# Kernel tuning notes

Hardware: AMD Instinct MI355X
Metric: run time of the kernel (lower is better)

## Reference

```python
import jax, jax.numpy as jnp
import numpy as np

B, T, D = 2, 2048, 2048
H, K, Hd = 16, 8, 128
EPS = 1e-6
THETA = 1e6


def _rms_norm(x, w):
    # x: [..., Hd]
    return x * jax.lax.rsqrt(jnp.mean(x * x, axis=-1, keepdims=True) + EPS) * w


def _rope(x, sin, cos):
    # x: [B, T, Hh, Hd]; sin/cos: [T, Hd//2]
    s = sin[None, :, None, :]
    c = cos[None, :, None, :]
    x1 = x[..., 0::2]
    x2 = x[..., 1::2]
    # NOTE: source concatenates halves (non-interleaved output), replicate exactly
    return jnp.concatenate([x1 * c - x2 * s, x1 * s + x2 * c], axis=-1)


def setup_inputs() -> dict:
    key = jax.random.key(0)
    ks = jax.random.split(key, 5)
    scale = 0.02
    x = jax.random.normal(ks[0], (B, T, D), dtype=jnp.float32)
    Wq = jax.random.normal(ks[1], (D, H * Hd), dtype=jnp.float32) * scale
    Wk = jax.random.normal(ks[2], (D, K * Hd), dtype=jnp.float32) * scale
    Wv = jax.random.normal(ks[3], (D, K * Hd), dtype=jnp.float32) * scale
    Wo = jax.random.normal(ks[4], (H * Hd, D), dtype=jnp.float32) * scale
    qn_w = jnp.ones((Hd,), dtype=jnp.float32)
    kn_w = jnp.ones((Hd,), dtype=jnp.float32)
    # RotaryEmbedding: inv_freq = theta**(-arange(0,Hd,2)/Hd); freqs = outer(t, inv_freq)
    inv_freq = 1.0 / (THETA ** (jnp.arange(0, Hd, 2, dtype=jnp.float32) / Hd))
    freqs = jnp.arange(T, dtype=jnp.float32)[:, None] * inv_freq[None, :]
    return {"x": x, "Wq": Wq, "Wk": Wk, "Wv": Wv, "Wo": Wo,
            "qn_w": qn_w, "kn_w": kn_w,
            "sin": jnp.sin(freqs), "cos": jnp.cos(freqs)}


def reference(x, Wq, Wk, Wv, Wo, qn_w, kn_w, sin, cos):
    Bx, Tx, _ = x.shape
    q = (x @ Wq).reshape(Bx, Tx, H, Hd)
    k = (x @ Wk).reshape(Bx, Tx, K, Hd)
    v = (x @ Wv).reshape(Bx, Tx, K, Hd)
    q = _rope(_rms_norm(q, qn_w), sin, cos)
    k = _rope(_rms_norm(k, kn_w), sin, cos)
    q = q.transpose(0, 2, 1, 3)  # [B,H,T,Hd]
    k = k.transpose(0, 2, 1, 3)  # [B,K,T,Hd]
    v = v.transpose(0, 2, 1, 3)
    if K != 1 and K != H:
        rep = H // K
        k = jnp.repeat(k, rep, axis=1)  # repeat_interleave on head dim
        v = jnp.repeat(v, rep, axis=1)
    att = jnp.einsum('bhqd,bhkd->bhqk', q.astype(jnp.float32),
                     k.astype(jnp.float32)) / np.sqrt(Hd).astype(np.float32)
    causal = jnp.tril(jnp.ones((Tx, Tx), dtype=bool))
    att = jnp.where(causal[None, None], att, -jnp.inf)
    att = jax.nn.softmax(att, axis=-1)
    out = jnp.einsum('bhqk,bhkd->bhqd', att, v.astype(jnp.float32))
    out = out.astype(q.dtype).transpose(0, 2, 1, 3).reshape(Bx, Tx, H * Hd)
    return out @ Wo
```

## Files before the change

kernel.cpp:

```cpp
#include <hip/hip_runtime.h>
#include <stdint.h>


#define B_ 2
#define T_ 2048
#define D_ 2048
#define H_ 16
#define KH_ 8
#define HD_ 128
#define M_ (B_*T_)
#define NQKV_ 4096
#define QK_SCALE_LOG2E 0.1275174337f

typedef unsigned short u16;
typedef unsigned int   u32;
typedef __attribute__((ext_vector_type(8)))  __bf16 bf16x8_t;
typedef __attribute__((ext_vector_type(4)))  float  f32x4_t;
typedef __attribute__((ext_vector_type(16))) float  f32x16_t;
typedef __attribute__((ext_vector_type(4)))  u32    u32x4_t;

__device__ __forceinline__ u16 f2bf(float f) {
    u32 x = __float_as_uint(f);
    return (u16)((x + 0x7fffu + ((x >> 16) & 1u)) >> 16);
}
__device__ __forceinline__ u32 pack2(u16 a, u16 b) { return (u32)a | ((u32)b << 16); }

__device__ __forceinline__ void gload16(const void* g, void* l) {
    __builtin_amdgcn_global_load_lds(
        (__attribute__((address_space(1))) const void*)(unsigned long long)g,
        (__attribute__((address_space(3))) void*)(u32)(unsigned long long)l,
        16, 0, 0);
}

__global__ void cast_x_kernel(const float* __restrict__ in, u16* __restrict__ out) {
    int i = (blockIdx.x * 256 + threadIdx.x) * 4;
    float4 v = *(const float4*)(in + i);
    u32 lo = pack2(f2bf(v.x), f2bf(v.y));
    u32 hi = pack2(f2bf(v.z), f2bf(v.w));
    *(uint2*)(out + i) = make_uint2(lo, hi);
}

__global__ void tcast_kernel(const float* __restrict__ in, u16* __restrict__ out,
                             int ncols) {
    __shared__ u16 tile[64][65];
    int k0 = blockIdx.x * 64;
    int n0 = blockIdx.y * 64;
    int tid = threadIdx.x;
#pragma unroll
    for (int i = 0; i < 8; ++i) {
        int idx = tid + i * 256;
        int r = idx >> 5, c2 = idx & 31;
        float2 v = *(const float2*)(in + (size_t)(k0 + r) * ncols + n0 + 2 * c2);
        tile[r][2 * c2]     = f2bf(v.x);
        tile[r][2 * c2 + 1] = f2bf(v.y);
    }
    __syncthreads();
#pragma unroll
    for (int i = 0; i < 8; ++i) {
        int idx = tid + i * 256;
        int rn = idx >> 5, c2 = idx & 31;
        *(u32*)(out + (size_t)(n0 + rn) * 2048 + k0 + 2 * c2) =
            pack2(tile[2 * c2][rn], tile[2 * c2 + 1][rn]);
    }
}

__global__ void __launch_bounds__(256)
gemm_kernel(const u16* __restrict__ A, const u16* __restrict__ Bt,
            float* __restrict__ C, int N) {
    __shared__ u16 As[128 * 32];
    __shared__ u16 Bs[128 * 32];
    const int tid  = threadIdx.x;
    const int lane = tid & 63;
    const int wid  = tid >> 6;
    const int m0 = blockIdx.x * 128;
    const int n0 = blockIdx.y * 128;

    const int c0 = wid * 2, c1 = wid * 2 + 1;
    const int r0 = c0 * 16 + (lane >> 2);
    const int r1 = c1 * 16 + (lane >> 2);
    const int cl = lane & 3;
    const int g0 = cl ^ ((r0 >> 1) & 3);
    const int g1 = cl ^ ((r1 >> 1) & 3);
    const u16* gA0 = A  + (size_t)(m0 + r0) * 2048 + g0 * 8;
    const u16* gA1 = A  + (size_t)(m0 + r1) * 2048 + g1 * 8;
    const u16* gB0 = Bt + (size_t)(n0 + r0) * 2048 + g0 * 8;
    const u16* gB1 = Bt + (size_t)(n0 + r1) * 2048 + g1 * 8;
    u16* lA0 = As + c0 * 512;
    u16* lA1 = As + c1 * 512;
    u16* lB0 = Bs + c0 * 512;
    u16* lB1 = Bs + c1 * 512;

    const int wm = (wid >> 1) * 64, wn = (wid & 1) * 64;
    const int fr  = lane & 15;
    const int kg  = lane >> 4;

    f32x4_t acc[4][4];
#pragma unroll
    for (int m = 0; m < 4; ++m)
#pragma unroll
        for (int n = 0; n < 4; ++n)
#pragma unroll
            for (int j = 0; j < 4; ++j) acc[m][n][j] = 0.0f;

    for (int ks = 0; ks < 64; ++ks) {
        gload16(gA0, lA0); gload16(gA1, lA1);
        gload16(gB0, lB0); gload16(gB1, lB1);
        gA0 += 32; gA1 += 32; gB0 += 32; gB1 += 32;
        __syncthreads();
        bf16x8_t af[4], bfv[4];
#pragma unroll
        for (int m = 0; m < 4; ++m) {
            int row = wm + m * 16 + fr;
            int phys = kg ^ ((row >> 1) & 3);
            af[m] = *(const bf16x8_t*)(As + row * 32 + phys * 8);
        }
#pragma unroll
        for (int n = 0; n < 4; ++n) {
            int row = wn + n * 16 + fr;
            int phys = kg ^ ((row >> 1) & 3);
            bfv[n] = *(const bf16x8_t*)(Bs + row * 32 + phys * 8);
        }
#pragma unroll
        for (int m = 0; m < 4; ++m)
#pragma unroll
            for (int n = 0; n < 4; ++n)
                acc[m][n] = __builtin_amdgcn_mfma_f32_16x16x32_bf16(
                    af[m], bfv[n], acc[m][n], 0, 0, 0);
        __syncthreads();
    }

#pragma unroll
    for (int m = 0; m < 4; ++m)
#pragma unroll
        for (int n = 0; n < 4; ++n) {
            int col   = n0 + wn + n * 16 + fr;
            int rbase = m0 + wm + m * 16 + kg * 4;
#pragma unroll
            for (int j = 0; j < 4; ++j)
                C[(size_t)(rbase + j) * N + col] = acc[m][n][j];
        }
}

__global__ void __launch_bounds__(256)
normrope_kernel(const float* __restrict__ Cqkv,
                const float* __restrict__ qw, const float* __restrict__ kw,
                const float* __restrict__ sinT, const float* __restrict__ cosT,
                u16* __restrict__ qbf, u16* __restrict__ kbf, u16* __restrict__ vbf) {
    int lane = threadIdx.x & 63;
    int w    = threadIdx.x >> 6;
    int rid  = blockIdx.x * 4 + w;
    int m   = rid >> 5;
    int sub = rid & 31;
    int b = m >> 11, t = m & (T_ - 1);

    if (sub >= 24) {
        int kh = sub - 24;
        float2 x = *(const float2*)(Cqkv + (size_t)m * NQKV_ + 3072 + kh * HD_ + 2 * lane);
        *(u32*)(vbf + ((size_t)(b * KH_ + kh) * T_ + t) * HD_ + 2 * lane) =
            pack2(f2bf(x.x), f2bf(x.y));
        return;
    }
    bool isq = sub < 16;
    int  hh  = isq ? sub : sub - 16;
    int  colbase = isq ? hh * HD_ : 2048 + hh * HD_;
    float2 x = *(const float2*)(Cqkv + (size_t)m * NQKV_ + colbase + 2 * lane);
    float ss = x.x * x.x + x.y * x.y;
#pragma unroll
    for (int sh = 1; sh < 64; sh <<= 1) ss += __shfl_xor(ss, sh, 64);
    float scale = rsqrtf(ss * (1.0f / 128.0f) + 1e-6f);
    const float* wp = isq ? qw : kw;
    float2 wv = *(const float2*)(wp + 2 * lane);
    float y1 = x.x * scale * wv.x;
    float y2 = x.y * scale * wv.y;
    float c = cosT[t * 64 + lane], s = sinT[t * 64 + lane];
    float oa = y1 * c - y2 * s;
    float ob = y1 * s + y2 * c;
    if (isq) { oa *= QK_SCALE_LOG2E; ob *= QK_SCALE_LOG2E; }
    u16* outp = isq ? (qbf + ((size_t)(b * H_  + hh) * T_ + t) * HD_)
                    : (kbf + ((size_t)(b * KH_ + hh) * T_ + t) * HD_);
    outp[lane]      = f2bf(oa);
    outp[64 + lane] = f2bf(ob);
}

__global__ void vtrans_kernel(const u16* __restrict__ in, u16* __restrict__ out) {
    __shared__ u16 tile[64][65];
    int t0 = blockIdx.x * 64;
    int d0 = blockIdx.y * 64;
    size_t bi = (size_t)blockIdx.z * T_ * HD_;
    size_t bo = (size_t)blockIdx.z * HD_ * T_;
    int tid = threadIdx.x;
#pragma unroll
    for (int i = 0; i < 8; ++i) {
        int idx = tid + i * 256;
        int r = idx >> 5, c2 = idx & 31;
        u32 v = *(const u32*)(in + bi + (size_t)(t0 + r) * HD_ + d0 + 2 * c2);
        tile[r][2 * c2]     = (u16)(v & 0xffffu);
        tile[r][2 * c2 + 1] = (u16)(v >> 16);
    }
    __syncthreads();
#pragma unroll
    for (int i = 0; i < 8; ++i) {
        int idx = tid + i * 256;
        int rd = idx >> 5, c2 = idx & 31;
        *(u32*)(out + bo + (size_t)(d0 + rd) * T_ + t0 + 2 * c2) =
            pack2(tile[2 * c2][rd], tile[2 * c2 + 1][rd]);
    }
}

__global__ void __launch_bounds__(256, 2)
attn_kernel(const u16* __restrict__ qg, const u16* __restrict__ kgl,
            const u16* __restrict__ vtg, u16* __restrict__ attout) {
    __shared__ u16 Kt[2][64 * 128];
    __shared__ u16 Vt[2][128 * 64];

    const int tid = threadIdx.x, lane = tid & 63, w = tid >> 6;
    const int qb = (int)gridDim.x - 1 - (int)blockIdx.x;
    const int h = blockIdx.y, b = blockIdx.z;
    const int kh = h >> 1;
    const int q0 = qb * 128;
    const int col = lane & 31;
    const int hi  = lane >> 5;
    const int l7  = lane & 7;
    const int l15 = lane & 15;
    const int qw0 = q0 + w * 32;
    const int qlane = qw0 + col;

    const u16* qbase = qg  + ((size_t)(b * H_  + h ) * T_) * HD_;
    const u16* kbase = kgl + ((size_t)(b * KH_ + kh) * T_) * HD_;
    const u16* vbase = vtg + ((size_t)(b * KH_ + kh) * HD_) * T_;

    bf16x8_t qf[8];
#pragma unroll
    for (int s = 0; s < 8; ++s)
        qf[s] = *(const bf16x8_t*)(qbase + (size_t)qlane * HD_ + s * 16 + hi * 8);

    const int krl = lane >> 4, kcl = lane & 15;
    const int vrl = lane >> 3, vcl = lane & 7;

    f32x16_t o[4];
#pragma unroll
    for (int dt = 0; dt < 4; ++dt)
#pragma unroll
        for (int r = 0; r < 16; ++r) o[dt][r] = 0.0f;
    float mrow = -1e30f, lrow = 0.0f;

    const int nt = 2 * (qb + 1);

#define STAGE(buf, tt)                                                          \
    do {                                                                        \
        int kv0s = (tt) * 64;                                                   \
        _Pragma("unroll")                                                       \
        for (int cc = 0; cc < 4; ++cc) {                                        \
            int c = w * 4 + cc;                                                 \
            int r = c * 4 + krl;                                                \
            gload16(kbase + (size_t)(kv0s + r) * HD_ + (kcl ^ (r & 15)) * 8,    \
                    &Kt[buf][c * 512]);                                         \
            int rv = c * 8 + vrl;                                               \
            gload16(vbase + (size_t)rv * T_ + kv0s + (vcl ^ (rv & 7)) * 8,      \
                    &Vt[buf][c * 512]);                                         \
        }                                                                       \
    } while (0)

    STAGE(0, 0);
    __syncthreads();

    for (int t = 0; t < nt; ++t) {
        const int cur = t & 1;
        const int kv0 = t * 64;
        if (t + 1 < nt) STAGE(cur ^ 1, t + 1);

        if (kv0 <= qw0 + 31) {
            f32x16_t s0, s1;
#pragma unroll
            for (int r = 0; r < 16; ++r) { s0[r] = 0.0f; s1[r] = 0.0f; }
            __builtin_amdgcn_s_setprio(1);
#pragma unroll
            for (int ss = 0; ss < 8; ++ss) {
                bf16x8_t kf0 = *(const bf16x8_t*)
                    (&Kt[cur][col * 128 + (((2 * ss + hi) ^ l15) * 8)]);
                s0 = __builtin_amdgcn_mfma_f32_32x32x16_bf16(kf0, qf[ss], s0, 0, 0, 0);
                bf16x8_t kf1 = *(const bf16x8_t*)
                    (&Kt[cur][(32 + col) * 128 + (((2 * ss + hi) ^ l15) * 8)]);
                s1 = __builtin_amdgcn_mfma_f32_32x32x16_bf16(kf1, qf[ss], s1, 0, 0, 0);
            }
            __builtin_amdgcn_s_setprio(0);
            if (kv0 + 63 > qw0) {
#pragma unroll
                for (int r = 0; r < 16; ++r) {
                    int cr = (r & 3) + 8 * (r >> 2) + 4 * hi;
                    if (kv0 + cr      > qlane) s0[r] = -1e30f;
                    if (kv0 + 32 + cr > qlane) s1[r] = -1e30f;
                }
            }
            float tmax = s0[0];
#pragma unroll
            for (int r = 1; r < 16; ++r) tmax = fmaxf(tmax, s0[r]);
#pragma unroll
            for (int r = 0; r < 16; ++r) tmax = fmaxf(tmax, s1[r]);
            tmax = fmaxf(tmax, __shfl_xor(tmax, 32, 64));
            float mnew = fmaxf(mrow, tmax);
            float corr = exp2f(mrow - mnew);
            mrow = mnew;
            float ps = 0.0f;
#pragma unroll
            for (int r = 0; r < 16; ++r) {
                s0[r] = exp2f(s0[r] - mrow); ps += s0[r];
                s1[r] = exp2f(s1[r] - mrow); ps += s1[r];
            }
            lrow = lrow * corr + ps;
#pragma unroll
            for (int dt = 0; dt < 4; ++dt)
#pragma unroll
                for (int r = 0; r < 16; ++r) o[dt][r] *= corr;
            u32 pd0[8], pd1[8], po0[8], po1[8];
#pragma unroll
            for (int i = 0; i < 8; ++i) {
                pd0[i] = pack2(f2bf(s0[2 * i]), f2bf(s0[2 * i + 1]));
                pd1[i] = pack2(f2bf(s1[2 * i]), f2bf(s1[2 * i + 1]));
                po0[i] = __shfl_xor(pd0[i], 32, 64);
                po1[i] = __shfl_xor(pd1[i], 32, 64);
            }
            bf16x8_t pf[4];
#pragma unroll
            for (int ks = 0; ks < 4; ++ks) {
                const u32* pd = (ks < 2) ? pd0 : pd1;
                const u32* po = (ks < 2) ? po0 : po1;
                int base = (ks & 1) * 4;
                union { u32 u[4]; bf16x8_t v; } f;
                f.u[0] = hi ? po[base + 2] : pd[base + 0];
                f.u[1] = hi ? po[base + 3] : pd[base + 1];
                f.u[2] = hi ? pd[base + 2] : po[base + 0];
                f.u[3] = hi ? pd[base + 3] : po[base + 1];
                pf[ks] = f.v;
            }
            __builtin_amdgcn_s_setprio(1);
#pragma unroll
            for (int dt = 0; dt < 4; ++dt) {
                int dl = dt * 32 + col;
#pragma unroll
                for (int ks = 0; ks < 4; ++ks) {
                    bf16x8_t vf = *(const bf16x8_t*)
                        (&Vt[cur][dl * 64 + (((2 * ks + hi) ^ l7) * 8)]);
                    o[dt] = __builtin_amdgcn_mfma_f32_32x32x16_bf16(vf, pf[ks], o[dt], 0, 0, 0);
                }
            }
            __builtin_amdgcn_s_setprio(0);
        }
        __syncthreads();
    }
#undef STAGE

    float ltot = lrow + __shfl_xor(lrow, 32, 64);
    float inv  = 1.0f / ltot;
    u16* Tr = &Kt[0][0] + w * 4096;
#pragma unroll
    for (int dt = 0; dt < 4; ++dt)
#pragma unroll
        for (int g = 0; g < 4; ++g) {
            int slot = ((dt << 2) | g) ^ (col & 7);
            u32 lo  = pack2(f2bf(o[dt][4 * g + 0] * inv), f2bf(o[dt][4 * g + 1] * inv));
            u32 hi2 = pack2(f2bf(o[dt][4 * g + 2] * inv), f2bf(o[dt][4 * g + 3] * inv));
            *(uint2*)(Tr + col * 128 + slot * 8 + 4 * hi) = make_uint2(lo, hi2);
        }
    size_t rowbase = (size_t)(b * T_ + qw0);
#pragma unroll
    for (int p = 0; p < 8; ++p) {
        int ql   = p * 4 + (lane >> 4);
        int slot = lane & 15;
        int dl   = (slot ^ (ql & 7)) * 8;
        u32x4_t v = *(const u32x4_t*)(Tr + ql * 128 + slot * 8);
        *(u32x4_t*)(attout + (rowbase + ql) * 2048 + h * HD_ + dl) = v;
    }
}

extern "C" void kernel_launch(void* const* d_in, const int* in_sizes, int n_in,
                              void* d_out, int out_size, void* d_ws, size_t ws_size,
                              hipStream_t stream) {
    const float* x    = (const float*)d_in[0];
    const float* Wq   = (const float*)d_in[1];
    const float* Wk   = (const float*)d_in[2];
    const float* Wv   = (const float*)d_in[3];
    const float* Wo   = (const float*)d_in[4];
    const float* qw   = (const float*)d_in[5];
    const float* kw   = (const float*)d_in[6];
    const float* sinT = (const float*)d_in[7];
    const float* cosT = (const float*)d_in[8];
    float* out = (float*)d_out;

    u16*  x_bf   = (u16*)d_ws;
    u16*  wqkv_t = x_bf   + (size_t)M_ * D_;
    u16*  wo_t   = wqkv_t + (size_t)4096 * 2048;
    float* c_qkv = (float*)(wo_t + (size_t)2048 * 2048);
    u16*  q_bf   = (u16*)(c_qkv + (size_t)M_ * NQKV_);
    u16*  k_bf   = q_bf + (size_t)B_ * H_  * T_ * HD_;
    u16*  v_bf   = k_bf + (size_t)B_ * KH_ * T_ * HD_;
    u16*  v_t    = v_bf + (size_t)B_ * KH_ * T_ * HD_;
    u16*  att_bf = v_t  + (size_t)B_ * KH_ * T_ * HD_;

    cast_x_kernel<<<(M_ * D_) / 1024, 256, 0, stream>>>(x, x_bf);
    tcast_kernel<<<dim3(32, 32), 256, 0, stream>>>(Wq, wqkv_t, 2048);
    tcast_kernel<<<dim3(32, 16), 256, 0, stream>>>(Wk, wqkv_t + (size_t)2048 * 2048, 1024);
    tcast_kernel<<<dim3(32, 16), 256, 0, stream>>>(Wv, wqkv_t + (size_t)3072 * 2048, 1024);
    tcast_kernel<<<dim3(32, 32), 256, 0, stream>>>(Wo, wo_t, 2048);

    gemm_kernel<<<dim3(32, 32), 256, 0, stream>>>(x_bf, wqkv_t, c_qkv, 4096);
    normrope_kernel<<<(M_ * 32) / 4, 256, 0, stream>>>(c_qkv, qw, kw, sinT, cosT,
                                                       q_bf, k_bf, v_bf);
    vtrans_kernel<<<dim3(32, 2, 16), 256, 0, stream>>>(v_bf, v_t);
    attn_kernel<<<dim3(16, 16, 2), 256, 0, stream>>>(q_bf, k_bf, v_t, att_bf);
    gemm_kernel<<<dim3(32, 16), 256, 0, stream>>>(att_bf, wo_t, out, 2048);
}
```

Before: 415.0 us.

## Replace GEMM with 256x256-tile 8-wave double-buffered pipelined kernel

Replaces the 128x128, single-buffered GEMM with a 256x256-tile, 512-thread kernel. It double-buffers A and B in LDS and splits each K step into four phases, so global loads for later tiles overlap with MFMA work, using sched barriers, s_setprio and explicit vmcnt waits. The larger tile raises data reuse per loaded byte and the deeper pipeline hides memory latency. The cost is much more LDS (128KB per block) and registers, lower occupancy, and far fewer blocks (256 and 128), which may underfill the GPU's compute units.

```diff
diff --git a/kernel.cpp b/kernel.cpp
--- a/kernel.cpp
+++ b/kernel.cpp
@@ -64,80 +64,140 @@
     }
 }
 
-__global__ void __launch_bounds__(256)
-gemm_kernel(const u16* __restrict__ A, const u16* __restrict__ Bt,
-            float* __restrict__ C, int N) {
-    __shared__ u16 As[128 * 32];
-    __shared__ u16 Bs[128 * 32];
+#define NKT 32
+
+__global__ void __launch_bounds__(512, 2)
+gemm8p_kernel(const u16* __restrict__ A, const u16* __restrict__ Bt,
+              float* __restrict__ C, int N) {
+    __shared__ u16 As[2][256 * 64];
+    __shared__ u16 Bs[2][256 * 64];
     const int tid  = threadIdx.x;
     const int lane = tid & 63;
-    const int wid  = tid >> 6;
-    const int m0 = blockIdx.x * 128;
-    const int n0 = blockIdx.y * 128;
-
-    const int c0 = wid * 2, c1 = wid * 2 + 1;
-    const int r0 = c0 * 16 + (lane >> 2);
-    const int r1 = c1 * 16 + (lane >> 2);
-    const int cl = lane & 3;
-    const int g0 = cl ^ ((r0 >> 1) & 3);
-    const int g1 = cl ^ ((r1 >> 1) & 3);
-    const u16* gA0 = A  + (size_t)(m0 + r0) * 2048 + g0 * 8;
-    const u16* gA1 = A  + (size_t)(m0 + r1) * 2048 + g1 * 8;
-    const u16* gB0 = Bt + (size_t)(n0 + r0) * 2048 + g0 * 8;
-    const u16* gB1 = Bt + (size_t)(n0 + r1) * 2048 + g1 * 8;
-    u16* lA0 = As + c0 * 512;
-    u16* lA1 = As + c1 * 512;
-    u16* lB0 = Bs + c0 * 512;
-    u16* lB1 = Bs + c1 * 512;
-
-    const int wm = (wid >> 1) * 64, wn = (wid & 1) * 64;
-    const int fr  = lane & 15;
-    const int kg  = lane >> 4;
-
-    f32x4_t acc[4][4];
-#pragma unroll
-    for (int m = 0; m < 4; ++m)
-#pragma unroll
-        for (int n = 0; n < 4; ++n)
-#pragma unroll
-            for (int j = 0; j < 4; ++j) acc[m][n][j] = 0.0f;
-
-    for (int ks = 0; ks < 64; ++ks) {
-        gload16(gA0, lA0); gload16(gA1, lA1);
-        gload16(gB0, lB0); gload16(gB1, lB1);
-        gA0 += 32; gA1 += 32; gB0 += 32; gB1 += 32;
-        __syncthreads();
-        bf16x8_t af[4], bfv[4];
-#pragma unroll
-        for (int m = 0; m < 4; ++m) {
-            int row = wm + m * 16 + fr;
-            int phys = kg ^ ((row >> 1) & 3);
-            af[m] = *(const bf16x8_t*)(As + row * 32 + phys * 8);
+    const int w    = tid >> 6;
+    const int wm   = w >> 2;
+    const int wn   = w & 3;
+    const int m0 = blockIdx.x * 256;
+    const int n0 = blockIdx.y * 256;
+    const int fr = lane & 15;
+    const int kg = lane >> 4;
+
+    const u16* Ag = A  + (size_t)m0 * 2048;
+    const u16* Bg = Bt + (size_t)n0 * 2048;
+
+#define STG(gbase, lbase, h, kt_)                                              \
+    do {                                                                       \
+        int _k0 = (kt_) * 64;                                                  \
+        _Pragma("unroll")                                                      \
+        for (int _i = 0; _i < 2; ++_i) {                                       \
+            int _r  = _i * 64 + w * 8 + (lane >> 3);                           \
+            int _sl = (lane & 7) ^ (_r & 7);                                   \
+            gload16((gbase) + (size_t)((h) * 128 + _r) * 2048 + _k0 + _sl * 8, \
+                    (lbase) + (h) * 8192 + (_i * 512 + w * 64) * 8);           \
+        }                                                                      \
+    } while (0)
+
+    bf16x8_t afr[4][2];
+    bf16x8_t bfr[2][2][2];
+    f32x4_t  acc[8][4];
+#pragma unroll
+    for (int i = 0; i < 8; ++i)
+#pragma unroll
+        for (int j = 0; j < 4; ++j)
+#pragma unroll
+            for (int e = 0; e < 4; ++e) acc[i][j][e] = 0.0f;
+
+#define RDA(qm)                                                                \
+    _Pragma("unroll")                                                          \
+    for (int _mf = 0; _mf < 4; ++_mf)                                          \
+        _Pragma("unroll")                                                      \
+        for (int _ks = 0; _ks < 2; ++_ks) {                                    \
+            int _row  = wm * 128 + ((qm) * 4 + _mf) * 16 + fr;                 \
+            int _phys = (_ks * 4 + kg) ^ (_row & 7);                           \
+            afr[_mf][_ks] = *(const bf16x8_t*)(Asc + _row * 64 + _phys * 8);   \
         }
-#pragma unroll
-        for (int n = 0; n < 4; ++n) {
-            int row = wn + n * 16 + fr;
-            int phys = kg ^ ((row >> 1) & 3);
-            bfv[n] = *(const bf16x8_t*)(Bs + row * 32 + phys * 8);
+#define RDB(qn)                                                                \
+    _Pragma("unroll")                                                          \
+    for (int _nf = 0; _nf < 2; ++_nf)                                          \
+        _Pragma("unroll")                                                      \
+        for (int _ks = 0; _ks < 2; ++_ks) {                                    \
+            int _row  = wn * 64 + ((qn) * 2 + _nf) * 16 + fr;                  \
+            int _phys = (_ks * 4 + kg) ^ (_row & 7);                           \
+            bfr[qn][_nf][_ks] = *(const bf16x8_t*)(Bsc + _row * 64 + _phys * 8);\
         }
-#pragma unroll
-        for (int m = 0; m < 4; ++m)
-#pragma unroll
-            for (int n = 0; n < 4; ++n)
-                acc[m][n] = __builtin_amdgcn_mfma_f32_16x16x32_bf16(
-                    af[m], bfv[n], acc[m][n], 0, 0, 0);
-        __syncthreads();
-    }
-
-#pragma unroll
-    for (int m = 0; m < 4; ++m)
-#pragma unroll
-        for (int n = 0; n < 4; ++n) {
-            int col   = n0 + wn + n * 16 + fr;
-            int rbase = m0 + wm + m * 16 + kg * 4;
+#define MM(qm, qn)                                                             \
+    _Pragma("unroll")                                                          \
+    for (int _mf = 0; _mf < 4; ++_mf)                                          \
+        _Pragma("unroll")                                                      \
+        for (int _nf = 0; _nf < 2; ++_nf)                                      \
+            _Pragma("unroll")                                                  \
+            for (int _ks = 0; _ks < 2; ++_ks)                                  \
+                acc[(qm) * 4 + _mf][(qn) * 2 + _nf] =                          \
+                    __builtin_amdgcn_mfma_f32_16x16x32_bf16(                   \
+                        afr[_mf][_ks], bfr[qn][_nf][_ks],                      \
+                        acc[(qm) * 4 + _mf][(qn) * 2 + _nf], 0, 0, 0);
+
+#define SBAR __builtin_amdgcn_sched_barrier(0)
+#define PH_MID                                                                 \
+    SBAR; __builtin_amdgcn_s_barrier();                                        \
+    asm volatile("s_waitcnt lgkmcnt(0)" ::: "memory"); SBAR;                   \
+    __builtin_amdgcn_s_setprio(1)
+#define PH_END                                                                 \
+    __builtin_amdgcn_s_setprio(0); SBAR;                                       \
+    __builtin_amdgcn_s_barrier(); SBAR
+
+    STG(Ag, &As[0][0], 0, 0);
+    STG(Ag, &As[0][0], 1, 0);
+    STG(Bg, &Bs[0][0], 0, 0);
+    STG(Bg, &Bs[0][0], 1, 0);
+    STG(Bg, &Bs[1][0], 0, 1);
+    STG(Bg, &Bs[1][0], 1, 1);
+    asm volatile("s_waitcnt vmcnt(4)" ::: "memory");
+    SBAR;
+    __builtin_amdgcn_s_barrier();
+    SBAR;
+
+    for (int kt = 0; kt < NKT; ++kt) {
+        const int cur = kt & 1;
+        const u16* Asc = &As[cur][0];
+        const u16* Bsc = &Bs[cur][0];
+        u16* Aso = &As[cur ^ 1][0];
+        u16* Bsw = &Bs[cur][0];
+        RDA(0); RDB(0);
+        if (kt + 1 < NKT) STG(Ag, Aso, 0, kt + 1);
+        PH_MID; MM(0, 0); PH_END;
+        RDB(1);
+        if (kt + 1 < NKT) STG(Ag, Aso, 1, kt + 1);
+        PH_MID; MM(0, 1); PH_END;
+        RDA(1);
+        if (kt + 2 < NKT) STG(Bg, Bsw, 0, kt + 2);
+        PH_MID; MM(1, 0); PH_END;
+        if (kt + 2 < NKT) STG(Bg, Bsw, 1, kt + 2);
+        SBAR; __builtin_amdgcn_s_barrier(); SBAR;
+        __builtin_amdgcn_s_setprio(1);
+        MM(1, 1);
+        __builtin_amdgcn_s_setprio(0); SBAR;
+        if (kt < NKT - 2) asm volatile("s_waitcnt vmcnt(4)" ::: "memory");
+        else              asm volatile("s_waitcnt vmcnt(0)" ::: "memory");
+        SBAR;
+        __builtin_amdgcn_s_barrier();
+        SBAR;
+    }
+#undef STG
+#undef RDA
+#undef RDB
+#undef MM
+#undef PH_MID
+#undef PH_END
+
+#pragma unroll
+    for (int mf = 0; mf < 8; ++mf)
+#pragma unroll
+        for (int nf = 0; nf < 4; ++nf) {
+            int colx  = n0 + wn * 64 + nf * 16 + fr;
+            int rbase = m0 + wm * 128 + mf * 16 + kg * 4;
 #pragma unroll
             for (int j = 0; j < 4; ++j)
-                C[(size_t)(rbase + j) * N + col] = acc[m][n][j];
+                C[(size_t)(rbase + j) * N + colx] = acc[mf][nf][j];
         }
 }
 
@@ -403,10 +463,10 @@
     tcast_kernel<<<dim3(32, 16), 256, 0, stream>>>(Wv, wqkv_t + (size_t)3072 * 2048, 1024);
     tcast_kernel<<<dim3(32, 32), 256, 0, stream>>>(Wo, wo_t, 2048);
 
-    gemm_kernel<<<dim3(32, 32), 256, 0, stream>>>(x_bf, wqkv_t, c_qkv, 4096);
+    gemm8p_kernel<<<dim3(16, 16), 512, 0, stream>>>(x_bf, wqkv_t, c_qkv, 4096);
     normrope_kernel<<<(M_ * 32) / 4, 256, 0, stream>>>(c_qkv, qw, kw, sinT, cosT,
                                                        q_bf, k_bf, v_bf);
     vtrans_kernel<<<dim3(32, 2, 16), 256, 0, stream>>>(v_bf, v_t);
     attn_kernel<<<dim3(16, 16, 2), 256, 0, stream>>>(q_bf, k_bf, v_t, att_bf);
-    gemm_kernel<<<dim3(32, 16), 256, 0, stream>>>(att_bf, wo_t, out, 2048);
-}
+    gemm8p_kernel<<<dim3(16, 8), 512, 0, stream>>>(att_bf, wo_t, out, 2048);
+}
```

Result: faster. 397.3 us (-4.3%).
